# Kernel optimization log

Hardware: AMD Instinct MI355X
Metric: run time of the kernel (lower is better)

Reference implementation:

```python
import jax, jax.numpy as jnp
from jax import lax
import numpy as np

B, S_DEC, S_ENC = 32, 128, 128
V, E, H = 32000, 200, 128


def setup_inputs() -> dict:
    key = jax.random.key(0)
    ks = jax.random.split(key, 10)
    emb = jax.random.normal(ks[0], (V, E), dtype=jnp.float32)
    emb = emb.at[0].set(0.0)  # padding_idx row (char2id[' '] -> 0)
    return {
        "sequence": jax.random.randint(ks[1], (B, S_DEC), 0, V),
        "hs": jax.random.normal(ks[2], (B, S_ENC, H), dtype=jnp.float32),
        "h": jax.random.normal(ks[3], (1, B, H), dtype=jnp.float32),
        "emb": emb,
        "w_ih": jax.random.normal(ks[4], (3 * H, E), dtype=jnp.float32) * 0.05,
        "w_hh": jax.random.normal(ks[5], (3 * H, H), dtype=jnp.float32) * 0.05,
        "b_ih": jax.random.normal(ks[6], (3 * H,), dtype=jnp.float32) * 0.05,
        "b_hh": jax.random.normal(ks[7], (3 * H,), dtype=jnp.float32) * 0.05,
        "w_out": jax.random.normal(ks[8], (V, 2 * H), dtype=jnp.float32) * 0.05,
        "b_out": jax.random.normal(ks[9], (V,), dtype=jnp.float32) * 0.05,
    }


def _gru(x_gates, h0, w_hh, b_hh):
    # x_gates: [B, S, 3H] precomputed input projections; torch gate order r,z,n
    def step(hprev, xg):
        hg = hprev @ w_hh.T + b_hh
        xr, xz, xn = jnp.split(xg, 3, axis=-1)
        hr, hz, hn = jnp.split(hg, 3, axis=-1)
        r = jax.nn.sigmoid(xr + hr)
        z = jax.nn.sigmoid(xz + hz)
        n = jnp.tanh(xn + r * hn)
        hnew = (1.0 - z) * n + z * hprev
        return hnew, hnew

    hT, outs = lax.scan(step, h0, jnp.swapaxes(x_gates, 0, 1))  # scan over time
    return jnp.swapaxes(outs, 0, 1), hT  # [B,S,H], [B,H]


def reference(sequence, hs, h, emb, w_ih, w_hh, b_ih, b_hh, w_out, b_out):
    # Embedding lookup (padding row already zero)
    x = emb[sequence]  # [B, S_dec, E]
    x_gates = jnp.einsum("bse,ge->bsg", x, w_ih) + b_ih  # [B, S_dec, 3H]
    output, hT = _gru(x_gates, h[0], w_hh, b_hh)  # [B, S_dec, H]
    state = hT[None]  # [1, B, H]
    # s = bmm(hs, output^T): [B, S_enc, S_dec]; softmax over encoder axis (dim=1)
    s = jnp.einsum("beh,bdh->bed", hs, output)
    attention_weight = jax.nn.softmax(s, axis=1)
    # context: replaces the per-timestep python loop with one contraction
    c = jnp.einsum("bed,beh->bdh", attention_weight, hs)  # [B, S_dec, H]
    cat = jnp.concatenate([output, c], axis=-1)  # [B, S_dec, 2H]
    logits = jnp.einsum("bdh,vh->bdv", cat, w_out) + b_out  # [B, S_dec, V]
    return logits, state, attention_weight
```

## Files before the change

kernel.cpp:

```cpp
#include <hip/hip_runtime.h>
#include <hip/hip_bf16.h>

#define B_    32
#define SDEC  128
#define SENC  128
#define V_    32000
#define E_    200
#define H_    128
#define G3    384

typedef __attribute__((ext_vector_type(8))) short bf16x8;
typedef __attribute__((ext_vector_type(4))) float f32x4;
typedef __attribute__((ext_vector_type(2))) float f32x2;

#define GLOBAL_AS __attribute__((address_space(1)))
#define LDS_AS    __attribute__((address_space(3)))

__device__ __forceinline__ float fast_sigmoid(float x) {
  return 1.f / (1.f + __expf(-x));
}
__device__ __forceinline__ float fast_tanh(float x) {
  float e2 = __expf(2.f * x);
  return 1.f - 2.f / (e2 + 1.f);
}
__device__ __forceinline__ float quad_reduce(float x) {
  int i = __builtin_bit_cast(int, x);
  int a = __builtin_amdgcn_mov_dpp(i, 0xB1, 0xF, 0xF, true);
  float s = x + __builtin_bit_cast(float, a);
  int j = __builtin_bit_cast(int, s);
  int c = __builtin_amdgcn_mov_dpp(j, 0x4E, 0xF, 0xF, true);
  return s + __builtin_bit_cast(float, c);
}

__global__ __launch_bounds__(192) void k_embed_proj(
    const int* __restrict__ seq, const float* __restrict__ emb,
    const float* __restrict__ w_ih, const float* __restrict__ b_ih,
    float* __restrict__ xg) {
  __shared__ __align__(16) float xs[16][E_];
  __shared__ int sidx[16];
  const int r0 = blockIdx.x * 16;
  const int t = threadIdx.x;
  if (t < 16) sidx[t] = seq[r0 + t];
  __syncthreads();
  for (int i = t; i < 800; i += 192) {
    int r = i / 50, c = i - r * 50;
    *(float4*)&xs[r][c * 4] =
        *(const float4*)(emb + (size_t)sidx[r] * E_ + c * 4);
  }
  __syncthreads();
  const int g0 = t, g1 = t + 192;
  float a0[16], a1[16];
#pragma unroll
  for (int r = 0; r < 16; r++) { a0[r] = 0.f; a1[r] = 0.f; }
  const float* w0 = w_ih + (size_t)g0 * E_;
  const float* w1 = w_ih + (size_t)g1 * E_;
  for (int k = 0; k < E_; k += 4) {
    float4 wv0 = *(const float4*)(w0 + k);
    float4 wv1 = *(const float4*)(w1 + k);
#pragma unroll
    for (int r = 0; r < 16; r++) {
      float4 xv = *(const float4*)&xs[r][k];
      a0[r] += wv0.x * xv.x + wv0.y * xv.y + wv0.z * xv.z + wv0.w * xv.w;
      a1[r] += wv1.x * xv.x + wv1.y * xv.y + wv1.z * xv.z + wv1.w * xv.w;
    }
  }
  const float b0 = b_ih[g0], b1 = b_ih[g1];
#pragma unroll
  for (int r = 0; r < 16; r++) {
    xg[(size_t)(r0 + r) * G3 + g0] = a0[r] + b0;
    xg[(size_t)(r0 + r) * G3 + g1] = a1[r] + b1;
  }
}

__global__ __launch_bounds__(512) void k_gru_attn_cvt(
    const float* __restrict__ xg, const float* __restrict__ h0,
    const float* __restrict__ w_hh, const float* __restrict__ b_hh,
    const float* __restrict__ hs, __hip_bfloat16* __restrict__ cat_bf,
    float* __restrict__ state_out, float* __restrict__ attw_out,
    const float* __restrict__ w_out, __hip_bfloat16* __restrict__ wout_bf) {
  if (blockIdx.x >= 32) {
    int idx = ((blockIdx.x - 32) * 512 + threadIdx.x) * 8;
    float4 a = *(const float4*)(w_out + idx);
    float4 c = *(const float4*)(w_out + idx + 4);
    union { __hip_bfloat16 h[8]; uint4 v; } p;
    p.h[0] = __float2bfloat16(a.x); p.h[1] = __float2bfloat16(a.y);
    p.h[2] = __float2bfloat16(a.z); p.h[3] = __float2bfloat16(a.w);
    p.h[4] = __float2bfloat16(c.x); p.h[5] = __float2bfloat16(c.y);
    p.h[6] = __float2bfloat16(c.z); p.h[7] = __float2bfloat16(c.w);
    *(uint4*)(wout_bf + idx) = p.v;
    return;
  }

  __shared__ __hip_bfloat16 ctb[128][128];
  __shared__ __hip_bfloat16 hsb[128][128];
  __shared__ __hip_bfloat16 hsT[128][128];
  __shared__ __align__(16) float hp[2][H_];

  const int b = blockIdx.x;
  const int t = threadIdx.x;
  const int hh = t >> 2;
  const int sub = t & 3;

  float wr_[32], wz_[32], wn_[32];
#pragma unroll
  for (int m = 0; m < 8; m++) {
    int c = (m + sub * 2) & 7;
    int kb = sub * 32 + c * 4;
    *(float4*)&wr_[m * 4] = *(const float4*)(w_hh + (size_t)hh * H_ + kb);
    *(float4*)&wz_[m * 4] = *(const float4*)(w_hh + (size_t)(128 + hh) * H_ + kb);
    *(float4*)&wn_[m * 4] = *(const float4*)(w_hh + (size_t)(256 + hh) * H_ + kb);
  }

  const float* xgb = xg + (size_t)b * SDEC * G3;
  const float br = b_hh[hh], bz = b_hh[128 + hh], bn = b_hh[256 + hh];
  float cxr = xgb[hh], cxz = xgb[128 + hh], cxn = xgb[256 + hh];
  if (t < H_) hp[0][t] = h0[b * H_ + t];
  __hip_bfloat16* catbfb = cat_bf + (size_t)b * SDEC * 256;

  asm volatile("s_waitcnt lgkmcnt(0)" ::: "memory");
  __builtin_amdgcn_s_barrier();
  asm volatile("" ::: "memory");

  int cur = 0;
  for (int s = 0; s < SDEC; s++) {
    float nxr = 0.f, nxz = 0.f, nxn = 0.f;
    if (s + 1 < SDEC) {
      const float* xp = xgb + (size_t)(s + 1) * G3;
      nxr = xp[hh]; nxz = xp[128 + hh]; nxn = xp[256 + hh];
    }
    f32x2 sr2 = {0.f, 0.f}, sz2 = {0.f, 0.f}, sn2 = {0.f, 0.f};
#pragma unroll
    for (int m = 0; m < 8; m++) {
      int c = (m + sub * 2) & 7;
      float4 hv = *(const float4*)&hp[cur][sub * 32 + c * 4];
      f32x2 h01 = {hv.x, hv.y}, h23 = {hv.z, hv.w};
      const f32x2* w2r = (const f32x2*)&wr_[m * 4];
      const f32x2* w2z = (const f32x2*)&wz_[m * 4];
      const f32x2* w2n = (const f32x2*)&wn_[m * 4];
      sr2 += w2r[0] * h01; sr2 += w2r[1] * h23;
      sz2 += w2z[0] * h01; sz2 += w2z[1] * h23;
      sn2 += w2n[0] * h01; sn2 += w2n[1] * h23;
    }
    float sr = quad_reduce(sr2[0] + sr2[1]);
    float sz = quad_reduce(sz2[0] + sz2[1]);
    float sn = quad_reduce(sn2[0] + sn2[1]);

    float hold = hp[cur][hh];
    float r = fast_sigmoid(cxr + sr + br);
    float z = fast_sigmoid(cxz + sz + bz);
    float n = fast_tanh(cxn + r * (sn + bn));
    float hnew = (1.f - z) * n + z * hold;
    if (sub == 0) {
      __hip_bfloat16 hb = __float2bfloat16(hnew);
      hp[cur ^ 1][hh] = hnew;
      catbfb[(size_t)s * 256 + hh] = hb;
      ctb[s][((hh >> 3) ^ (s & 7)) * 8 + (hh & 7)] = hb;
    }
    asm volatile("s_waitcnt lgkmcnt(0)" ::: "memory");
    __builtin_amdgcn_s_barrier();
    asm volatile("" ::: "memory");
    cur ^= 1;
    cxr = nxr; cxz = nxz; cxn = nxn;
  }

  const int w = t >> 6, l = t & 63;
  const int lr = l & 15, lk = l >> 4;
  const float* hsbase = hs + (size_t)b * SENC * H_;

  for (int i = t; i < 2048; i += 512) {
    int e = i >> 4, c = i & 15;
    float4 v0 = *(const float4*)(hsbase + e * H_ + c * 8);
    float4 v1 = *(const float4*)(hsbase + e * H_ + c * 8 + 4);
    union { __hip_bfloat16 h[8]; uint4 u; } pk;
    pk.h[0] = __float2bfloat16(v0.x); pk.h[1] = __float2bfloat16(v0.y);
    pk.h[2] = __float2bfloat16(v0.z); pk.h[3] = __float2bfloat16(v0.w);
    pk.h[4] = __float2bfloat16(v1.x); pk.h[5] = __float2bfloat16(v1.y);
    pk.h[6] = __float2bfloat16(v1.z); pk.h[7] = __float2bfloat16(v1.w);
    *(uint4*)&hsb[e][((c ^ (e & 7)) * 8)] = pk.u;
  }
  if (t < H_) state_out[b * H_ + t] = hp[cur][t];
  __syncthreads();

  for (int i = t; i < 2048; i += 512) {
    int c = i >> 7, e = i & 127;
    uint4 v = *(const uint4*)&hsb[e][((c ^ (e & 7)) * 8)];
    const __hip_bfloat16* hv = (const __hip_bfloat16*)&v;
#pragma unroll
    for (int u = 0; u < 8; u++) {
      int h = c * 8 + u;
      int col = (e + 8 * (h & 15)) & 127;
      hsT[h][col] = hv[u];
    }
  }
  const int d = w * 16 + lr;
  bf16x8 afrag[4];
#pragma unroll
  for (int kt = 0; kt < 4; kt++)
    afrag[kt] = *(const bf16x8*)&ctb[d][(((kt * 4 + lk) ^ (lr & 7)) * 8)];
  __syncthreads();

  f32x4 acc[8];
#pragma unroll
  for (int et = 0; et < 8; et++) acc[et] = (f32x4){0.f, 0.f, 0.f, 0.f};
#pragma unroll
  for (int et = 0; et < 8; et++) {
#pragma unroll
    for (int kt = 0; kt < 4; kt++) {
      bf16x8 bfrag =
          *(const bf16x8*)&hsb[et * 16 + lr][(((kt * 4 + lk) ^ (lr & 7)) * 8)];
      acc[et] =
          __builtin_amdgcn_mfma_f32_16x16x32_bf16(bfrag, afrag[kt], acc[et], 0, 0, 0);
    }
  }

  float mx = -1e30f;
#pragma unroll
  for (int et = 0; et < 8; et++)
    mx = fmaxf(mx, fmaxf(fmaxf(acc[et][0], acc[et][1]),
                         fmaxf(acc[et][2], acc[et][3])));
  mx = fmaxf(mx, __shfl_xor(mx, 16));
  mx = fmaxf(mx, __shfl_xor(mx, 32));
  float sum = 0.f;
#pragma unroll
  for (int et = 0; et < 8; et++) {
    acc[et][0] = __expf(acc[et][0] - mx);
    acc[et][1] = __expf(acc[et][1] - mx);
    acc[et][2] = __expf(acc[et][2] - mx);
    acc[et][3] = __expf(acc[et][3] - mx);
    sum += acc[et][0] + acc[et][1] + acc[et][2] + acc[et][3];
  }
  sum += __shfl_xor(sum, 16);
  sum += __shfl_xor(sum, 32);
  const float inv = 1.f / sum;

  __hip_bfloat16 (*plds)[128] = ctb;
  float* aw = attw_out + (size_t)b * SENC * SDEC + d;
#pragma unroll
  for (int et = 0; et < 8; et++) {
    acc[et][0] *= inv; acc[et][1] *= inv;
    acc[et][2] *= inv; acc[et][3] *= inv;
    union { __hip_bfloat16 h[4]; uint2 u; } pk4;
    pk4.h[0] = __float2bfloat16(acc[et][0]);
    pk4.h[1] = __float2bfloat16(acc[et][1]);
    pk4.h[2] = __float2bfloat16(acc[et][2]);
    pk4.h[3] = __float2bfloat16(acc[et][3]);
    *(uint2*)&plds[d][(((et * 2 + (lk >> 1)) ^ (lr & 7)) * 8 + 4 * (lk & 1))] =
        pk4.u;
    const int e0 = et * 16 + lk * 4;
#pragma unroll
    for (int j = 0; j < 4; j++)
      aw[(size_t)(e0 + j) * SDEC] = acc[et][j];
  }
  __syncthreads();

  bf16x8 pfrag[4];
#pragma unroll
  for (int f = 0; f < 4; f++)
    pfrag[f] = *(const bf16x8*)&plds[d][(((f * 4 + lk) ^ (lr & 7)) * 8)];
#pragma unroll
  for (int ht = 0; ht < 8; ht++) {
    f32x4 a2 = (f32x4){0.f, 0.f, 0.f, 0.f};
#pragma unroll
    for (int kt = 0; kt < 4; kt++) {
      bf16x8 hfrag =
          *(const bf16x8*)&hsT[ht * 16 + lr][((kt * 32 + lk * 8 + 8 * lr) & 127)];
      a2 = __builtin_amdgcn_mfma_f32_16x16x32_bf16(hfrag, pfrag[kt], a2, 0, 0, 0);
    }
    union { __hip_bfloat16 h[4]; uint2 u; } pk4;
    pk4.h[0] = __float2bfloat16(a2[0]);
    pk4.h[1] = __float2bfloat16(a2[1]);
    pk4.h[2] = __float2bfloat16(a2[2]);
    pk4.h[3] = __float2bfloat16(a2[3]);
    *(uint2*)(cat_bf + (size_t)(b * SDEC + d) * 256 + 128 + ht * 16 + lk * 4) =
        pk4.u;
  }
}

__global__ __launch_bounds__(512) void k_gemm_mfma(
    const __hip_bfloat16* __restrict__ A, const __hip_bfloat16* __restrict__ Bw,
    const float* __restrict__ b_out, float* __restrict__ C) {
  constexpr int K = 256, N = V_, Kt = 32;
  alignas(16) __shared__ char smem[73728];
  __hip_bfloat16 (*As)[4096] = (__hip_bfloat16(*)[4096])smem;
  __hip_bfloat16 (*Bs)[8192] = (__hip_bfloat16(*)[8192])(smem + 24576);
  float* tr = (float*)smem;

  const int tid = threadIdx.x;
  const int w = tid >> 6, l = tid & 63;
  const int wr = w >> 2, wc = w & 3;
  const int lr = l & 15, lk = l >> 4;
  const int lq = l >> 2, lc = l & 3;

  const int bid = blockIdx.x;
  const int wgid = (bid & 7) * 500 + (bid >> 3);
  const int mt = wgid & 31;
  const int nt = wgid >> 5;
  const int m0 = mt * 128, n0 = nt * 256;

  f32x4 acc[4][4];
#pragma unroll
  for (int m = 0; m < 4; m++)
#pragma unroll
    for (int n = 0; n < 4; n++) acc[m][n] = (f32x4){0.f, 0.f, 0.f, 0.f};

#define STAGE(buf, kk)                                                            \
  do {                                                                            \
    const __hip_bfloat16* gA = A + (size_t)(m0 + w * 16 + lq) * K + (kk) + lc * 8;\
    const __hip_bfloat16* gB0 = Bw + (size_t)(n0 + w * 32 + lq) * K + (kk) + lc * 8;\
    const __hip_bfloat16* gB1 = gB0 + (size_t)16 * K;                             \
    __builtin_amdgcn_global_load_lds((const GLOBAL_AS void*)gA,                   \
        (LDS_AS void*)(&As[buf][w * 512]), 16, 0, 0);                             \
    __builtin_amdgcn_global_load_lds((const GLOBAL_AS void*)gB0,                  \
        (LDS_AS void*)(&Bs[buf][w * 1024]), 16, 0, 0);                            \
    __builtin_amdgcn_global_load_lds((const GLOBAL_AS void*)gB1,                  \
        (LDS_AS void*)(&Bs[buf][w * 1024 + 512]), 16, 0, 0);                      \
  } while (0)

  STAGE(0, 0);
  STAGE(1, Kt);

#pragma unroll
  for (int t = 0; t < 8; ++t) {
    if (t < 7) asm volatile("s_waitcnt vmcnt(3)" ::: "memory");
    else       asm volatile("s_waitcnt vmcnt(0)" ::: "memory");
    __builtin_amdgcn_s_barrier();
    asm volatile("" ::: "memory");

    const int c = t % 3;
    bf16x8 af[4], bfr[4];
#pragma unroll
    for (int m = 0; m < 4; m++)
      af[m] = *(const bf16x8*)(const void*)(&As[c][(wr * 64 + m * 16 + lr) * Kt + lk * 8]);
#pragma unroll
    for (int n = 0; n < 4; n++)
      bfr[n] = *(const bf16x8*)(const void*)(&Bs[c][(wc * 64 + n * 16 + lr) * Kt + lk * 8]);

    if (t < 6) STAGE((t + 2) % 3, (t + 2) * Kt);

#pragma unroll
    for (int m = 0; m < 4; m++)
#pragma unroll
      for (int n = 0; n < 4; n++)
        acc[m][n] = __builtin_amdgcn_mfma_f32_16x16x32_bf16(bfr[n], af[m], acc[m][n], 0, 0, 0);
  }
#undef STAGE

  __syncthreads();
#pragma unroll
  for (int h = 0; h < 2; ++h) {
    if (wr == h) {
#pragma unroll
      for (int m = 0; m < 4; m++) {
#pragma unroll
        for (int n = 0; n < 4; n++) {
          const int row = m * 16 + lr;
          const int col = wc * 64 + n * 16 + lk * 4;
          const float4 bo = *(const float4*)(b_out + n0 + col);
          f32x4 v;
          v[0] = acc[m][n][0] + bo.x;
          v[1] = acc[m][n][1] + bo.y;
          v[2] = acc[m][n][2] + bo.z;
          v[3] = acc[m][n][3] + bo.w;
          *(f32x4*)&tr[row * 260 + col] = v;
        }
      }
    }
    __syncthreads();
#pragma unroll
    for (int i = 0; i < 8; ++i) {
      const int c2 = i * 512 + tid;
      const int row = c2 >> 6;
      const int off = (c2 & 63) * 4;
      f32x4 v = *(const f32x4*)&tr[row * 260 + off];
      __builtin_nontemporal_store(
          v, (f32x4*)(C + (size_t)(m0 + h * 64 + row) * N + n0 + off));
    }
    __syncthreads();
  }
}

extern "C" void kernel_launch(void* const* d_in, const int* in_sizes, int n_in,
                              void* d_out, int out_size, void* d_ws, size_t ws_size,
                              hipStream_t stream) {
  const int* seq = (const int*)d_in[0];
  const float* hs = (const float*)d_in[1];
  const float* h0 = (const float*)d_in[2];
  const float* emb = (const float*)d_in[3];
  const float* w_ih = (const float*)d_in[4];
  const float* w_hh = (const float*)d_in[5];
  const float* b_ih = (const float*)d_in[6];
  const float* b_hh = (const float*)d_in[7];
  const float* w_out = (const float*)d_in[8];
  const float* b_out = (const float*)d_in[9];

  float* out = (float*)d_out;
  float* logits = out;
  float* state = out + 131072000;
  float* attw = out + 131072000 + 4096;

  char* ws = (char*)d_ws;
  float* xg = (float*)ws;
  __hip_bfloat16* cat_bf = (__hip_bfloat16*)(ws + 10485760);
  __hip_bfloat16* wout_bf = (__hip_bfloat16*)(ws + 12582912);

  k_embed_proj<<<256, 192, 0, stream>>>(seq, emb, w_ih, b_ih, xg);
  k_gru_attn_cvt<<<2032, 512, 0, stream>>>(xg, h0, w_hh, b_hh, hs, cat_bf,
                                           state, attw, w_out, wout_bf);
  k_gemm_mfma<<<4000, 512, 0, stream>>>(cat_bf, wout_bf, b_out, logits);
}
```

Before: 251.8 us.

## Shrink GEMM LDS to double buffering, chunk epilogue, coarsen weight conversion

Result: slower. 292.3 us (+16.1%).

```diff
diff --git a/kernel.cpp b/kernel.cpp
--- a/kernel.cpp
+++ b/kernel.cpp
@@ -79,15 +79,19 @@
     float* __restrict__ state_out, float* __restrict__ attw_out,
     const float* __restrict__ w_out, __hip_bfloat16* __restrict__ wout_bf) {
   if (blockIdx.x >= 32) {
-    int idx = ((blockIdx.x - 32) * 512 + threadIdx.x) * 8;
-    float4 a = *(const float4*)(w_out + idx);
-    float4 c = *(const float4*)(w_out + idx + 4);
-    union { __hip_bfloat16 h[8]; uint4 v; } p;
-    p.h[0] = __float2bfloat16(a.x); p.h[1] = __float2bfloat16(a.y);
-    p.h[2] = __float2bfloat16(a.z); p.h[3] = __float2bfloat16(a.w);
-    p.h[4] = __float2bfloat16(c.x); p.h[5] = __float2bfloat16(c.y);
-    p.h[6] = __float2bfloat16(c.z); p.h[7] = __float2bfloat16(c.w);
-    *(uint4*)(wout_bf + idx) = p.v;
+    const int base = (blockIdx.x - 32) * 4;
+#pragma unroll
+    for (int j = 0; j < 4; j++) {
+      int idx = ((base + j) * 512 + threadIdx.x) * 8;
+      float4 a = *(const float4*)(w_out + idx);
+      float4 c = *(const float4*)(w_out + idx + 4);
+      union { __hip_bfloat16 h[8]; uint4 v; } p;
+      p.h[0] = __float2bfloat16(a.x); p.h[1] = __float2bfloat16(a.y);
+      p.h[2] = __float2bfloat16(a.z); p.h[3] = __float2bfloat16(a.w);
+      p.h[4] = __float2bfloat16(c.x); p.h[5] = __float2bfloat16(c.y);
+      p.h[6] = __float2bfloat16(c.z); p.h[7] = __float2bfloat16(c.w);
+      *(uint4*)(wout_bf + idx) = p.v;
+    }
     return;
   }
 
@@ -280,9 +284,9 @@
     const __hip_bfloat16* __restrict__ A, const __hip_bfloat16* __restrict__ Bw,
     const float* __restrict__ b_out, float* __restrict__ C) {
   constexpr int K = 256, N = V_, Kt = 32;
-  alignas(16) __shared__ char smem[73728];
+  alignas(16) __shared__ char smem[49152];
   __hip_bfloat16 (*As)[4096] = (__hip_bfloat16(*)[4096])smem;
-  __hip_bfloat16 (*Bs)[8192] = (__hip_bfloat16(*)[8192])(smem + 24576);
+  __hip_bfloat16 (*Bs)[8192] = (__hip_bfloat16(*)[8192])(smem + 16384);
   float* tr = (float*)smem;
 
   const int tid = threadIdx.x;
@@ -326,7 +330,7 @@
     __builtin_amdgcn_s_barrier();
     asm volatile("" ::: "memory");
 
-    const int c = t % 3;
+    const int c = t & 1;
     bf16x8 af[4], bfr[4];
 #pragma unroll
     for (int m = 0; m < 4; m++)
@@ -335,45 +339,57 @@
     for (int n = 0; n < 4; n++)
       bfr[n] = *(const bf16x8*)(const void*)(&Bs[c][(wc * 64 + n * 16 + lr) * Kt + lk * 8]);
 
-    if (t < 6) STAGE((t + 2) % 3, (t + 2) * Kt);
-
+    asm volatile("s_waitcnt lgkmcnt(0)" ::: "memory");
+    __builtin_amdgcn_s_barrier();
+    asm volatile("" ::: "memory");
+
+    if (t < 6) STAGE(c, (t + 2) * Kt);
+
+    __builtin_amdgcn_s_setprio(1);
 #pragma unroll
     for (int m = 0; m < 4; m++)
 #pragma unroll
       for (int n = 0; n < 4; n++)
         acc[m][n] = __builtin_amdgcn_mfma_f32_16x16x32_bf16(bfr[n], af[m], acc[m][n], 0, 0, 0);
+    __builtin_amdgcn_s_setprio(0);
   }
 #undef STAGE
 
-  __syncthreads();
-#pragma unroll
-  for (int h = 0; h < 2; ++h) {
-    if (wr == h) {
-#pragma unroll
-      for (int m = 0; m < 4; m++) {
+  float4 bo_n[4];
+#pragma unroll
+  for (int n = 0; n < 4; n++)
+    bo_n[n] = *(const float4*)(b_out + n0 + wc * 64 + n * 16 + lk * 4);
+
+  __syncthreads();
+#pragma unroll
+  for (int q = 0; q < 4; ++q) {
+    if (wr == (q >> 1)) {
+      const int mbase = 2 * (q & 1);
+#pragma unroll
+      for (int mm = 0; mm < 2; mm++) {
+        const int m = mbase + mm;
+        const int row = mm * 16 + lr;
 #pragma unroll
         for (int n = 0; n < 4; n++) {
-          const int row = m * 16 + lr;
           const int col = wc * 64 + n * 16 + lk * 4;
-          const float4 bo = *(const float4*)(b_out + n0 + col);
           f32x4 v;
-          v[0] = acc[m][n][0] + bo.x;
-          v[1] = acc[m][n][1] + bo.y;
-          v[2] = acc[m][n][2] + bo.z;
-          v[3] = acc[m][n][3] + bo.w;
+          v[0] = acc[m][n][0] + bo_n[n].x;
+          v[1] = acc[m][n][1] + bo_n[n].y;
+          v[2] = acc[m][n][2] + bo_n[n].z;
+          v[3] = acc[m][n][3] + bo_n[n].w;
           *(f32x4*)&tr[row * 260 + col] = v;
         }
       }
     }
     __syncthreads();
 #pragma unroll
-    for (int i = 0; i < 8; ++i) {
+    for (int i = 0; i < 4; ++i) {
       const int c2 = i * 512 + tid;
       const int row = c2 >> 6;
       const int off = (c2 & 63) * 4;
       f32x4 v = *(const f32x4*)&tr[row * 260 + off];
       __builtin_nontemporal_store(
-          v, (f32x4*)(C + (size_t)(m0 + h * 64 + row) * N + n0 + off));
+          v, (f32x4*)(C + (size_t)(m0 + q * 32 + row) * N + n0 + off));
     }
     __syncthreads();
   }
@@ -404,7 +420,7 @@
   __hip_bfloat16* wout_bf = (__hip_bfloat16*)(ws + 12582912);
 
   k_embed_proj<<<256, 192, 0, stream>>>(seq, emb, w_ih, b_ih, xg);
-  k_gru_attn_cvt<<<2032, 512, 0, stream>>>(xg, h0, w_hh, b_hh, hs, cat_bf,
-                                           state, attw, w_out, wout_bf);
+  k_gru_attn_cvt<<<532, 512, 0, stream>>>(xg, h0, w_hh, b_hh, hs, cat_bf,
+                                          state, attw, w_out, wout_bf);
   k_gemm_mfma<<<4000, 512, 0, stream>>>(cat_bf, wout_bf, b_out, logits);
 }
```
